# Kernel optimization log

Hardware: AMD Instinct MI355X
Metric: run time of the kernel (lower is better)

Reference implementation:

```python
import jax, jax.numpy as jnp
import numpy as np

N_NODES = 50000
N_EDGES = 800000
X_DIM, H_DIM, Y_DIM = 128, 256, 128


def spmm(adj_vals, adj_row, adj_col, x):
    # sparse [N,N] @ dense [N,D] via gather + segment scatter-add
    msgs = adj_vals[:, None] * x[adj_col]  # [E, D]
    return jax.ops.segment_sum(msgs, adj_row, num_segments=N_NODES)


def setup_inputs() -> dict:
    key = jax.random.key(0)
    ks = jax.random.split(key, 6)
    x = jax.random.uniform(ks[0], (N_NODES, X_DIM), dtype=jnp.float32)
    adj_vals = jax.random.uniform(ks[1], (N_EDGES,), dtype=jnp.float32)
    adj_row = jax.random.randint(ks[2], (N_EDGES,), 0, N_NODES, dtype=jnp.int32)
    adj_col = jax.random.randint(ks[3], (N_EDGES,), 0, N_NODES, dtype=jnp.int32)
    W1 = jax.random.normal(ks[4], (X_DIM, H_DIM), dtype=jnp.float32) * (1.0 / np.sqrt(X_DIM))
    b1 = jnp.zeros((H_DIM,), dtype=jnp.float32)
    W2 = jax.random.normal(ks[5], (H_DIM, Y_DIM), dtype=jnp.float32) * (1.0 / np.sqrt(H_DIM))
    b2 = jnp.zeros((Y_DIM,), dtype=jnp.float32)
    return {"x": x, "adj_vals": adj_vals, "adj_row": adj_row, "adj_col": adj_col,
            "W1": W1, "b1": b1, "W2": W2, "b2": b2}


def reference(x, adj_vals, adj_row, adj_col, W1, b1, W2, b2):
    # row-normalize features: x / (sum_j x_ij + 1e-4)
    x = x / (jnp.sum(x, axis=1, keepdims=True) + 1e-4)
    # layer 1: spmm -> linear -> relu (dropout is identity at eval)
    h = jax.nn.relu(spmm(adj_vals, adj_row, adj_col, x) @ W1 + b1)  # [N, H]
    # layer 2: spmm -> linear
    y = spmm(adj_vals, adj_row, adj_col, h) @ W2 + b2  # [N, Y]
    return y
```

## Files before the change

### kernel.cpp

```cpp
#include <hip/hip_runtime.h>

#define N_NODES 50000
#define N_EDGES 800000
#define X_DIM 128
#define H_DIM 256
#define Y_DIM 128

typedef unsigned int uint32;
typedef unsigned short ushort16;
typedef __attribute__((ext_vector_type(8))) short short8;
typedef __attribute__((ext_vector_type(4))) float floatx4;

__device__ inline ushort16 f2bf(float f) {
    uint32 u = __float_as_uint(f);
    return (ushort16)((u + 0x7FFFu + ((u >> 16) & 1u)) >> 16);
}
__device__ inline float bf_lo(uint32 u) { return __uint_as_float(u << 16); }
__device__ inline float bf_hi(uint32 u) { return __uint_as_float(u & 0xFFFF0000u); }

#define BUCKET_SHIFT 7
#define NB 391
#define CHUNK 4096
#define NCHUNK 196
#define CAP_B 2560

#define NORM_BLOCKS 12500
#define CONV_BLOCKS 256

__global__ __launch_bounds__(256) void prep_kernel(
    const float* __restrict__ x, uint32* __restrict__ xb,
    const float* __restrict__ W1, const float* __restrict__ W2,
    ushort16* __restrict__ W1t, ushort16* __restrict__ W2t,
    const int* __restrict__ rows, int* __restrict__ gpartial) {
    int b = blockIdx.x;
    if (b < NORM_BLOCKS) {
        int row = (b * 256 + threadIdx.x) >> 6;
        int lane = threadIdx.x & 63;
        float2 v = ((const float2*)x)[(size_t)row * 64 + lane];
        float s = v.x + v.y;
        #pragma unroll
        for (int off = 32; off > 0; off >>= 1) s += __shfl_xor(s, off, 64);
        float inv = 1.0f / (s + 1e-4f);
        uint32 lo = (uint32)f2bf(v.x * inv);
        uint32 hi = (uint32)f2bf(v.y * inv);
        xb[(size_t)row * 64 + lane] = lo | (hi << 16);
    } else if (b < NORM_BLOCKS + CONV_BLOCKS) {
        int t = (b - NORM_BLOCKS) * 256 + threadIdx.x;
        if (t < X_DIM * H_DIM) {
            int n = t >> 7, k = t & 127;
            W1t[t] = f2bf(W1[k * H_DIM + n]);
        } else {
            int u = t - X_DIM * H_DIM;
            int y = u >> 8, k = u & 255;
            W2t[u] = f2bf(W2[k * Y_DIM + y]);
        }
    } else {
        __shared__ int h[NB];
        int j = b - NORM_BLOCKS - CONV_BLOCKS;
        int t = threadIdx.x;
        for (int i = t; i < NB; i += 256) h[i] = 0;
        __syncthreads();
        int base = j * CHUNK;
        #pragma unroll
        for (int k = 0; k < CHUNK / 256; k++) {
            int e = base + t + k * 256;
            if (e < N_EDGES) atomicAdd(&h[rows[e] >> BUCKET_SHIFT], 1);
        }
        __syncthreads();
        for (int i = t; i < NB; i += 256) gpartial[j * NB + i] = h[i];
    }
}

__global__ __launch_bounds__(512) void bucket_scan_kernel(
    const int* __restrict__ gpartial, int* __restrict__ bucket_base,
    int* __restrict__ bcursor, int* __restrict__ rowptr) {
    __shared__ int s[512];
    int t = threadIdx.x;
    int total = 0;
    if (t < NB) {
        #pragma unroll 4
        for (int j = 0; j < NCHUNK; j++) total += gpartial[j * NB + t];
    }
    s[t] = total;
    __syncthreads();
    #pragma unroll
    for (int off = 1; off < 512; off <<= 1) {
        int u = (t >= off) ? s[t - off] : 0;
        __syncthreads();
        s[t] += u;
        __syncthreads();
    }
    if (t < NB) {
        int excl = s[t] - total;
        bucket_base[t] = excl;
        bcursor[t] = excl;
    }
    if (t == 0) { bucket_base[NB] = N_EDGES; rowptr[N_NODES] = N_EDGES; }
}

__global__ __launch_bounds__(512) void bucketize_kernel(
    const int* __restrict__ rows, const int* __restrict__ cols,
    const float* __restrict__ vals, const int* __restrict__ gpartial,
    int* __restrict__ bcursor, int2* __restrict__ edges) {
    __shared__ int ob[512];
    __shared__ int c[NB];
    __shared__ int g[NB];
    __shared__ int2 buf[CHUNK];
    int t = threadIdx.x;
    int j = blockIdx.x;
    int base = j * CHUNK;
    int M = N_EDGES - base; if (M > CHUNK) M = CHUNK;
    int cnt = (t < NB) ? gpartial[j * NB + t] : 0;
    ob[t] = cnt;
    __syncthreads();
    #pragma unroll
    for (int off = 1; off < 512; off <<= 1) {
        int u = (t >= off) ? ob[t - off] : 0;
        __syncthreads();
        ob[t] += u;
        __syncthreads();
    }
    ob[t] -= cnt;
    if (t < NB) {
        c[t] = 0;
        g[t] = (cnt > 0) ? atomicAdd(&bcursor[t], cnt) : 0;
    }
    __syncthreads();
    #pragma unroll
    for (int k = 0; k < CHUNK / 512; k++) {
        int e = base + t + k * 512;
        if (e < N_EDGES) {
            int r = rows[e];
            int bb = r >> BUCKET_SHIFT;
            int p = ob[bb] + atomicAdd(&c[bb], 1);
            buf[p] = make_int2(cols[e] | ((r & 127) << 16) | (bb << 23),
                               __float_as_int(vals[e]));
        }
    }
    __syncthreads();
    for (int i = t; i < M; i += 512) {
        int2 e = buf[i];
        int bb = (int)((uint32)e.x >> 23);
        edges[g[bb] + (i - ob[bb])] = e;
    }
}

__global__ __launch_bounds__(256) void bucket_sort_kernel(
    const int* __restrict__ bucket_base, int2* __restrict__ edges,
    int2* __restrict__ scratch, int* __restrict__ rowptr) {
    __shared__ int2 buf[CAP_B];
    __shared__ int2 buf2[CAP_B];
    __shared__ int h[128], o[128], c[128];
    int b = blockIdx.x, t = threadIdx.x;
    int base = bucket_base[b];
    int cnt = bucket_base[b + 1] - base;
    bool fits = (cnt <= CAP_B);
    if (t < 128) h[t] = 0;
    __syncthreads();
    for (int i = t; i < cnt; i += 256) {
        int2 e = edges[base + i];
        if (fits) buf[i] = e; else scratch[base + i] = e;
        atomicAdd(&h[(e.x >> 16) & 127], 1);
    }
    __syncthreads();
    int valh = (t < 128) ? h[t] : 0;
    #pragma unroll
    for (int off = 1; off < 128; off <<= 1) {
        int u = (t >= off && t < 128) ? h[t - off] : 0;
        __syncthreads();
        if (t < 128) h[t] += u;
        __syncthreads();
    }
    if (t < 128) {
        o[t] = h[t] - valh;
        c[t] = 0;
        int i = (b << BUCKET_SHIFT) + t;
        if (i < N_NODES) rowptr[i] = base + h[t] - valh;
    }
    __syncthreads();
    for (int i = t; i < cnt; i += 256) {
        int2 e = fits ? buf[i] : scratch[base + i];
        int lr = (e.x >> 16) & 127;
        int p = o[lr] + atomicAdd(&c[lr], 1);
        if (fits) buf2[p] = e; else edges[base + p] = e;
    }
    __syncthreads();
    if (fits)
        for (int i = t; i < cnt; i += 256) edges[base + i] = buf2[i];
}

__device__ __forceinline__ void spmm_row4(const uint4* __restrict__ feat4,
                                          const int2* __restrict__ edges,
                                          int start, int end, int lane,
                                          float A[8]) {
    const int g16 = lane & 15;
    const int bsrc = lane & 48;
    int cur = start;
    while (__any(cur < end)) {
        int n = end - cur;
        n = n < 0 ? 0 : (n > 16 ? 16 : n);
        int2 ev = make_int2(0, 0);
        if (g16 < n) ev = edges[cur + g16];
        int c = ev.x & 0xFFFF;
        float v = __int_as_float(ev.y);
        int n0 = __shfl(n, 0, 64), n1 = __shfl(n, 16, 64);
        int n2 = __shfl(n, 32, 64), n3 = __shfl(n, 48, 64);
        int nm = max(max(n0, n1), max(n2, n3));
        int jm = (nm + 7) & ~7;
        for (int j = 0; j < jm; j += 8) {
            uint4 f[8];
            float vv[8];
            #pragma unroll
            for (int u = 0; u < 8; u++) {
                int cc = __shfl(c, bsrc + j + u, 64);
                vv[u] = __shfl(v, bsrc + j + u, 64);
                f[u] = feat4[(size_t)cc * 16 + g16];
            }
            #pragma unroll
            for (int u = 0; u < 8; u++) {
                A[0] += vv[u] * bf_lo(f[u].x); A[1] += vv[u] * bf_hi(f[u].x);
                A[2] += vv[u] * bf_lo(f[u].y); A[3] += vv[u] * bf_hi(f[u].y);
                A[4] += vv[u] * bf_lo(f[u].z); A[5] += vv[u] * bf_hi(f[u].z);
                A[6] += vv[u] * bf_lo(f[u].w); A[7] += vv[u] * bf_hi(f[u].w);
            }
        }
        cur += n;
    }
}

__global__ __launch_bounds__(512, 4) void spmm_gemm_fused(
    const uint32* __restrict__ xb, const int* __restrict__ rowptr,
    const int2* __restrict__ edges, const ushort16* __restrict__ W1t,
    const ushort16* __restrict__ W2t, const float* __restrict__ b1,
    ushort16* __restrict__ hw) {
    __shared__ ushort16 a_s[64 * 136];
    __shared__ ushort16 h_s[64 * 264];
    const int tx = threadIdx.x;
    const int wave = tx >> 6, lane = tx & 63;
    const int quad = lane >> 4, l16 = lane & 15;
    const int row0 = blockIdx.x * 64;
    const uint4* xb4 = (const uint4*)xb;

    for (int i = 0; i < 2; i++) {
        int r = wave * 8 + i * 4 + quad;
        int row = row0 + r;
        int s = 0, e = 0;
        if (row < N_NODES) { s = rowptr[row]; e = rowptr[row + 1]; }
        float A[8] = {0.f, 0.f, 0.f, 0.f, 0.f, 0.f, 0.f, 0.f};
        spmm_row4(xb4, edges, s, e, lane, A);
        uint4 pk;
        pk.x = (uint32)f2bf(A[0]) | ((uint32)f2bf(A[1]) << 16);
        pk.y = (uint32)f2bf(A[2]) | ((uint32)f2bf(A[3]) << 16);
        pk.z = (uint32)f2bf(A[4]) | ((uint32)f2bf(A[5]) << 16);
        pk.w = (uint32)f2bf(A[6]) | ((uint32)f2bf(A[7]) << 16);
        *(uint4*)&a_s[r * 136 + l16 * 8] = pk;
    }

    short8 bfr1[2][4];
    #pragma unroll
    for (int ct = 0; ct < 2; ct++)
        #pragma unroll
        for (int kk = 0; kk < 4; kk++)
            bfr1[ct][kk] = *(const short8*)
                &W1t[(wave * 32 + ct * 16 + l16) * 128 + kk * 32 + quad * 8];
    __syncthreads();

    floatx4 acc1[4][2];
    #pragma unroll
    for (int rs = 0; rs < 4; rs++)
        #pragma unroll
        for (int ct = 0; ct < 2; ct++)
            #pragma unroll
            for (int j = 0; j < 4; j++) acc1[rs][ct][j] = 0.f;
    #pragma unroll
    for (int kk = 0; kk < 4; kk++) {
        #pragma unroll
        for (int rs = 0; rs < 4; rs++) {
            short8 af = *(const short8*)&a_s[(rs * 16 + l16) * 136 + kk * 32 + quad * 8];
            #pragma unroll
            for (int ct = 0; ct < 2; ct++)
                acc1[rs][ct] = __builtin_amdgcn_mfma_f32_16x16x32_bf16(
                    af, bfr1[ct][kk], acc1[rs][ct], 0, 0, 0);
        }
    }
    float bv[2];
    #pragma unroll
    for (int ct = 0; ct < 2; ct++) bv[ct] = b1[wave * 32 + ct * 16 + l16];
    #pragma unroll
    for (int rs = 0; rs < 4; rs++)
        #pragma unroll
        for (int ct = 0; ct < 2; ct++)
            #pragma unroll
            for (int reg = 0; reg < 4; reg++) {
                float v = acc1[rs][ct][reg] + bv[ct];
                v = v > 0.f ? v : 0.f;
                h_s[(rs * 16 + quad * 4 + reg) * 264 + wave * 32 + ct * 16 + l16] = f2bf(v);
            }

    short8 bfr2[8];
    #pragma unroll
    for (int kk = 0; kk < 8; kk++)
        bfr2[kk] = *(const short8*)
            &W2t[(wave * 16 + l16) * 256 + kk * 32 + quad * 8];
    __syncthreads();

    floatx4 acc2[4];
    #pragma unroll
    for (int rs = 0; rs < 4; rs++)
        #pragma unroll
        for (int j = 0; j < 4; j++) acc2[rs][j] = 0.f;
    #pragma unroll
    for (int kk = 0; kk < 8; kk++) {
        #pragma unroll
        for (int rs = 0; rs < 4; rs++) {
            short8 af = *(const short8*)&h_s[(rs * 16 + l16) * 264 + kk * 32 + quad * 8];
            acc2[rs] = __builtin_amdgcn_mfma_f32_16x16x32_bf16(
                af, bfr2[kk], acc2[rs], 0, 0, 0);
        }
    }
    #pragma unroll
    for (int rs = 0; rs < 4; rs++)
        #pragma unroll
        for (int reg = 0; reg < 4; reg++) {
            int row = row0 + rs * 16 + quad * 4 + reg;
            if (row < N_NODES)
                hw[(size_t)row * 128 + wave * 16 + l16] = f2bf(acc2[rs][reg]);
        }
}

__global__ __launch_bounds__(256) void spmm_out_kernel(
    const uint32* __restrict__ feat, const int* __restrict__ rowptr,
    const int2* __restrict__ edges, const float* __restrict__ bias,
    float* __restrict__ out) {
    int w = (blockIdx.x * blockDim.x + threadIdx.x) >> 6;
    int lane = threadIdx.x & 63;
    int quad = lane >> 4, g16 = lane & 15;
    int row = w * 4 + quad;
    int s = rowptr[row], e = rowptr[row + 1];
    float A[8] = {0.f, 0.f, 0.f, 0.f, 0.f, 0.f, 0.f, 0.f};
    spmm_row4((const uint4*)feat, edges, s, e, lane, A);
    float4 b0 = ((const float4*)bias)[g16 * 2];
    float4 b1 = ((const float4*)bias)[g16 * 2 + 1];
    ((float4*)out)[(size_t)row * 32 + g16 * 2] =
        make_float4(A[0] + b0.x, A[1] + b0.y, A[2] + b0.z, A[3] + b0.w);
    ((float4*)out)[(size_t)row * 32 + g16 * 2 + 1] =
        make_float4(A[4] + b1.x, A[5] + b1.y, A[6] + b1.z, A[7] + b1.w);
}

extern "C" void kernel_launch(void* const* d_in, const int* in_sizes, int n_in,
                              void* d_out, int out_size, void* d_ws, size_t ws_size,
                              hipStream_t stream) {
    const float* x = (const float*)d_in[0];
    const float* adj_vals = (const float*)d_in[1];
    const int* adj_row = (const int*)d_in[2];
    const int* adj_col = (const int*)d_in[3];
    const float* W1 = (const float*)d_in[4];
    const float* b1 = (const float*)d_in[5];
    const float* W2 = (const float*)d_in[6];
    const float* b2 = (const float*)d_in[7];
    float* out = (float*)d_out;

    char* ws = (char*)d_ws;
    uint32*   xb       = (uint32*)  (ws + 0);
    ushort16* hw       = (ushort16*)(ws + 12800000);
    int2*     edges    = (int2*)    (ws + 25600000);
    int2*     scratch  = (int2*)    (ws + 32000000);
    int*      gpartial = (int*)     (ws + 38400000);
    int*      rowptr   = (int*)     (ws + 38713344);
    int*      bbase    = (int*)     (ws + 38914048);
    int*      bcursor  = (int*)     (ws + 38916096);
    ushort16* W1t      = (ushort16*)(ws + 38918144);
    ushort16* W2t      = (ushort16*)(ws + 38983680);

    hipLaunchKernelGGL(prep_kernel, dim3(NORM_BLOCKS + CONV_BLOCKS + NCHUNK),
                       dim3(256), 0, stream, x, xb, W1, W2, W1t, W2t,
                       adj_row, gpartial);

    hipLaunchKernelGGL(bucket_scan_kernel, dim3(1), dim3(512),
                       0, stream, gpartial, bbase, bcursor, rowptr);

    hipLaunchKernelGGL(bucketize_kernel, dim3(NCHUNK), dim3(512),
                       0, stream, adj_row, adj_col, adj_vals, gpartial, bcursor, edges);
    hipLaunchKernelGGL(bucket_sort_kernel, dim3(NB), dim3(256),
                       0, stream, bbase, edges, scratch, rowptr);

    hipLaunchKernelGGL(spmm_gemm_fused, dim3((N_NODES + 63) / 64), dim3(512),
                       0, stream, xb, rowptr, edges, W1t, W2t, b1, hw);

    hipLaunchKernelGGL(spmm_out_kernel, dim3(N_NODES / 16), dim3(256),
                       0, stream, (const uint32*)hw, rowptr, edges, b2, out);
}
```

Measured before the change: 208.2 us.

## Fold bucket scan into bucketize and split fused SpMM-GEMM into two kernels

Removes the single-block bucket_scan kernel. Each bucketize block now recomputes global bucket totals and its own per-chunk prefix from gpartial, so no global atomic cursor is needed. It also splits the fused layer-1 SpMM+GEMM kernel into a high-occupancy SpMM kernel (256 threads, 8 blocks per CU) that writes a bf16 aggregate to global memory, followed by a GEMM kernel that reads it. The goal is to drop a serial launch and let the gather-bound SpMM run at higher occupancy. The cost is an extra global round trip for the 50000x128 aggregate and redundant reads of gpartial in every bucketize block. Scratch now aliases the hw buffer.

```diff
diff --git a/kernel.cpp b/kernel.cpp
--- a/kernel.cpp
+++ b/kernel.cpp
@@ -71,68 +71,64 @@
     }
 }
 
-__global__ __launch_bounds__(512) void bucket_scan_kernel(
-    const int* __restrict__ gpartial, int* __restrict__ bucket_base,
-    int* __restrict__ bcursor, int* __restrict__ rowptr) {
-    __shared__ int s[512];
-    int t = threadIdx.x;
-    int total = 0;
-    if (t < NB) {
-        #pragma unroll 4
-        for (int j = 0; j < NCHUNK; j++) total += gpartial[j * NB + t];
-    }
-    s[t] = total;
-    __syncthreads();
-    #pragma unroll
-    for (int off = 1; off < 512; off <<= 1) {
-        int u = (t >= off) ? s[t - off] : 0;
-        __syncthreads();
-        s[t] += u;
-        __syncthreads();
-    }
-    if (t < NB) {
-        int excl = s[t] - total;
-        bucket_base[t] = excl;
-        bcursor[t] = excl;
-    }
-    if (t == 0) { bucket_base[NB] = N_EDGES; rowptr[N_NODES] = N_EDGES; }
-}
-
 __global__ __launch_bounds__(512) void bucketize_kernel(
     const int* __restrict__ rows, const int* __restrict__ cols,
     const float* __restrict__ vals, const int* __restrict__ gpartial,
-    int* __restrict__ bcursor, int2* __restrict__ edges) {
+    int2* __restrict__ edges, int* __restrict__ bucket_base,
+    int* __restrict__ rowptr) {
+    __shared__ int sc[512];
     __shared__ int ob[512];
-    __shared__ int c[NB];
-    __shared__ int g[NB];
+    __shared__ int gw[NB];
+    __shared__ int cur[NB];
     __shared__ int2 buf[CHUNK];
     int t = threadIdx.x;
     int j = blockIdx.x;
     int base = j * CHUNK;
     int M = N_EDGES - base; if (M > CHUNK) M = CHUNK;
-    int cnt = (t < NB) ? gpartial[j * NB + t] : 0;
-    ob[t] = cnt;
+
+    int total = 0, pre = 0, cnt = 0;
+    if (t < NB) {
+        for (int jj = 0; jj < NCHUNK; jj++) {
+            int v = gpartial[jj * NB + t];
+            total += v;
+            pre += (jj < j) ? v : 0;
+        }
+        cnt = gpartial[j * NB + t];
+    }
+    sc[t] = total;
     __syncthreads();
     #pragma unroll
     for (int off = 1; off < 512; off <<= 1) {
-        int u = (t >= off) ? ob[t - off] : 0;
-        __syncthreads();
-        ob[t] += u;
-        __syncthreads();
-    }
-    ob[t] -= cnt;
-    if (t < NB) {
-        c[t] = 0;
-        g[t] = (cnt > 0) ? atomicAdd(&bcursor[t], cnt) : 0;
-    }
-    __syncthreads();
+        int u = (t >= off) ? sc[t - off] : 0;
+        __syncthreads();
+        sc[t] += u;
+        __syncthreads();
+    }
+    int bexcl = sc[t] - total;
+    if (t < NB) { gw[t] = bexcl + pre; cur[t] = 0; }
+    if (j == 0) {
+        if (t < NB) bucket_base[t] = bexcl;
+        if (t == 0) { bucket_base[NB] = N_EDGES; rowptr[N_NODES] = N_EDGES; }
+    }
+    sc[t] = cnt;
+    __syncthreads();
+    #pragma unroll
+    for (int off = 1; off < 512; off <<= 1) {
+        int u = (t >= off) ? sc[t - off] : 0;
+        __syncthreads();
+        sc[t] += u;
+        __syncthreads();
+    }
+    ob[t] = sc[t] - cnt;
+    __syncthreads();
+
     #pragma unroll
     for (int k = 0; k < CHUNK / 512; k++) {
         int e = base + t + k * 512;
         if (e < N_EDGES) {
             int r = rows[e];
             int bb = r >> BUCKET_SHIFT;
-            int p = ob[bb] + atomicAdd(&c[bb], 1);
+            int p = ob[bb] + atomicAdd(&cur[bb], 1);
             buf[p] = make_int2(cols[e] | ((r & 127) << 16) | (bb << 23),
                                __float_as_int(vals[e]));
         }
@@ -141,7 +137,7 @@
     for (int i = t; i < M; i += 512) {
         int2 e = buf[i];
         int bb = (int)((uint32)e.x >> 23);
-        edges[g[bb] + (i - ob[bb])] = e;
+        edges[gw[bb] + (i - ob[bb])] = e;
     }
 }
 
@@ -228,33 +224,33 @@
     }
 }
 
-__global__ __launch_bounds__(512, 4) void spmm_gemm_fused(
+__global__ __launch_bounds__(256, 8) void spmm1_kernel(
     const uint32* __restrict__ xb, const int* __restrict__ rowptr,
-    const int2* __restrict__ edges, const ushort16* __restrict__ W1t,
+    const int2* __restrict__ edges, uint32* __restrict__ agg) {
+    int w = (blockIdx.x * blockDim.x + threadIdx.x) >> 6;
+    int lane = threadIdx.x & 63;
+    int quad = lane >> 4, g16 = lane & 15;
+    int row = w * 4 + quad;
+    int s = rowptr[row], e = rowptr[row + 1];
+    float A[8] = {0.f, 0.f, 0.f, 0.f, 0.f, 0.f, 0.f, 0.f};
+    spmm_row4((const uint4*)xb, edges, s, e, lane, A);
+    uint4 pk;
+    pk.x = (uint32)f2bf(A[0]) | ((uint32)f2bf(A[1]) << 16);
+    pk.y = (uint32)f2bf(A[2]) | ((uint32)f2bf(A[3]) << 16);
+    pk.z = (uint32)f2bf(A[4]) | ((uint32)f2bf(A[5]) << 16);
+    pk.w = (uint32)f2bf(A[6]) | ((uint32)f2bf(A[7]) << 16);
+    ((uint4*)agg)[(size_t)row * 16 + g16] = pk;
+}
+
+__global__ __launch_bounds__(512, 4) void gemm_kernel(
+    const ushort16* __restrict__ agg, const ushort16* __restrict__ W1t,
     const ushort16* __restrict__ W2t, const float* __restrict__ b1,
     ushort16* __restrict__ hw) {
-    __shared__ ushort16 a_s[64 * 136];
     __shared__ ushort16 h_s[64 * 264];
     const int tx = threadIdx.x;
     const int wave = tx >> 6, lane = tx & 63;
     const int quad = lane >> 4, l16 = lane & 15;
     const int row0 = blockIdx.x * 64;
-    const uint4* xb4 = (const uint4*)xb;
-
-    for (int i = 0; i < 2; i++) {
-        int r = wave * 8 + i * 4 + quad;
-        int row = row0 + r;
-        int s = 0, e = 0;
-        if (row < N_NODES) { s = rowptr[row]; e = rowptr[row + 1]; }
-        float A[8] = {0.f, 0.f, 0.f, 0.f, 0.f, 0.f, 0.f, 0.f};
-        spmm_row4(xb4, edges, s, e, lane, A);
-        uint4 pk;
-        pk.x = (uint32)f2bf(A[0]) | ((uint32)f2bf(A[1]) << 16);
-        pk.y = (uint32)f2bf(A[2]) | ((uint32)f2bf(A[3]) << 16);
-        pk.z = (uint32)f2bf(A[4]) | ((uint32)f2bf(A[5]) << 16);
-        pk.w = (uint32)f2bf(A[6]) | ((uint32)f2bf(A[7]) << 16);
-        *(uint4*)&a_s[r * 136 + l16 * 8] = pk;
-    }
 
     short8 bfr1[2][4];
     #pragma unroll
@@ -263,7 +259,6 @@
         for (int kk = 0; kk < 4; kk++)
             bfr1[ct][kk] = *(const short8*)
                 &W1t[(wave * 32 + ct * 16 + l16) * 128 + kk * 32 + quad * 8];
-    __syncthreads();
 
     floatx4 acc1[4][2];
     #pragma unroll
@@ -276,7 +271,10 @@
     for (int kk = 0; kk < 4; kk++) {
         #pragma unroll
         for (int rs = 0; rs < 4; rs++) {
-            short8 af = *(const short8*)&a_s[(rs * 16 + l16) * 136 + kk * 32 + quad * 8];
+            int row = row0 + rs * 16 + l16;
+            short8 af = {};
+            if (row < N_NODES)
+                af = *(const short8*)&agg[(size_t)row * 128 + kk * 32 + quad * 8];
             #pragma unroll
             for (int ct = 0; ct < 2; ct++)
                 acc1[rs][ct] = __builtin_amdgcn_mfma_f32_16x16x32_bf16(
@@ -363,29 +361,31 @@
     char* ws = (char*)d_ws;
     uint32*   xb       = (uint32*)  (ws + 0);
     ushort16* hw       = (ushort16*)(ws + 12800000);
+    int2*     scratch  = (int2*)    (ws + 12800000);
     int2*     edges    = (int2*)    (ws + 25600000);
-    int2*     scratch  = (int2*)    (ws + 32000000);
-    int*      gpartial = (int*)     (ws + 38400000);
-    int*      rowptr   = (int*)     (ws + 38713344);
-    int*      bbase    = (int*)     (ws + 38914048);
-    int*      bcursor  = (int*)     (ws + 38916096);
-    ushort16* W1t      = (ushort16*)(ws + 38918144);
-    ushort16* W2t      = (ushort16*)(ws + 38983680);
+    ushort16* agg      = (ushort16*)(ws + 32000000);
+    int*      gpartial = (int*)     (ws + 44800000);
+    int*      rowptr   = (int*)     (ws + 45106560);
+    int*      bbase    = (int*)     (ws + 45306624);
+    ushort16* W1t      = (ushort16*)(ws + 45308224);
+    ushort16* W2t      = (ushort16*)(ws + 45373760);
 
     hipLaunchKernelGGL(prep_kernel, dim3(NORM_BLOCKS + CONV_BLOCKS + NCHUNK),
                        dim3(256), 0, stream, x, xb, W1, W2, W1t, W2t,
                        adj_row, gpartial);
 
-    hipLaunchKernelGGL(bucket_scan_kernel, dim3(1), dim3(512),
-                       0, stream, gpartial, bbase, bcursor, rowptr);
-
     hipLaunchKernelGGL(bucketize_kernel, dim3(NCHUNK), dim3(512),
-                       0, stream, adj_row, adj_col, adj_vals, gpartial, bcursor, edges);
+                       0, stream, adj_row, adj_col, adj_vals, gpartial,
+                       edges, bbase, rowptr);
+
     hipLaunchKernelGGL(bucket_sort_kernel, dim3(NB), dim3(256),
                        0, stream, bbase, edges, scratch, rowptr);
 
-    hipLaunchKernelGGL(spmm_gemm_fused, dim3((N_NODES + 63) / 64), dim3(512),
-                       0, stream, xb, rowptr, edges, W1t, W2t, b1, hw);
+    hipLaunchKernelGGL(spmm1_kernel, dim3(N_NODES / 16), dim3(256),
+                       0, stream, xb, rowptr, edges, (uint32*)agg);
+
+    hipLaunchKernelGGL(gemm_kernel, dim3((N_NODES + 63) / 64), dim3(512),
+                       0, stream, agg, W1t, W2t, b1, hw);
 
     hipLaunchKernelGGL(spmm_out_kernel, dim3(N_NODES / 16), dim3(256),
                        0, stream, (const uint32*)hw, rowptr, edges, b2, out);
```

Result: slower. 300.7 us (+44.4%).

## Quantize normalized input features to 8-bit with per-row scales for first SpMM

Applied to the files above, without the earlier changes.

The prep kernel now quantizes each input row to uint8 using a per-row max-based scale, folding the row-normalization into a stored float scale. The first SpMM gathers 8-byte rows instead of 16-byte bf16 rows and multiplies each edge value by the source row's scale, which halves gather traffic in the fused layer-1 kernel at the cost of one extra scale load per edge and lower precision. The output SpMM also gets an occupancy hint in its launch bounds. The 8-bit precision loss may or may not stay within tolerance.

```diff
diff --git a/kernel.cpp b/kernel.cpp
--- a/kernel.cpp
+++ b/kernel.cpp
@@ -18,6 +18,11 @@
 __device__ inline float bf_lo(uint32 u) { return __uint_as_float(u << 16); }
 __device__ inline float bf_hi(uint32 u) { return __uint_as_float(u & 0xFFFF0000u); }
 
+__device__ inline float ub0(uint32 u) { return (float)(u & 0xFFu); }
+__device__ inline float ub1(uint32 u) { return (float)((u >> 8) & 0xFFu); }
+__device__ inline float ub2(uint32 u) { return (float)((u >> 16) & 0xFFu); }
+__device__ inline float ub3(uint32 u) { return (float)(u >> 24); }
+
 #define BUCKET_SHIFT 7
 #define NB 391
 #define CHUNK 4096
@@ -28,7 +33,8 @@
 #define CONV_BLOCKS 256
 
 __global__ __launch_bounds__(256) void prep_kernel(
-    const float* __restrict__ x, uint32* __restrict__ xb,
+    const float* __restrict__ x, unsigned short* __restrict__ xq,
+    float* __restrict__ scales,
     const float* __restrict__ W1, const float* __restrict__ W2,
     ushort16* __restrict__ W1t, ushort16* __restrict__ W2t,
     const int* __restrict__ rows, int* __restrict__ gpartial) {
@@ -38,12 +44,18 @@
         int lane = threadIdx.x & 63;
         float2 v = ((const float2*)x)[(size_t)row * 64 + lane];
         float s = v.x + v.y;
-        #pragma unroll
-        for (int off = 32; off > 0; off >>= 1) s += __shfl_xor(s, off, 64);
+        float m = fmaxf(v.x, v.y);
+        #pragma unroll
+        for (int off = 32; off > 0; off >>= 1) {
+            s += __shfl_xor(s, off, 64);
+            m = fmaxf(m, __shfl_xor(m, off, 64));
+        }
         float inv = 1.0f / (s + 1e-4f);
-        uint32 lo = (uint32)f2bf(v.x * inv);
-        uint32 hi = (uint32)f2bf(v.y * inv);
-        xb[(size_t)row * 64 + lane] = lo | (hi << 16);
+        float rq = (m > 0.f) ? 127.f / m : 0.f;
+        int q0 = (int)(v.x * rq + 0.5f);
+        int q1 = (int)(v.y * rq + 0.5f);
+        xq[(size_t)row * 64 + lane] = (unsigned short)(q0 | (q1 << 8));
+        if (lane == 0) scales[row] = m * inv * (1.f / 127.f);
     } else if (b < NORM_BLOCKS + CONV_BLOCKS) {
         int t = (b - NORM_BLOCKS) * 256 + threadIdx.x;
         if (t < X_DIM * H_DIM) {
@@ -187,6 +199,50 @@
     __syncthreads();
     if (fits)
         for (int i = t; i < cnt; i += 256) edges[base + i] = buf2[i];
+}
+
+__device__ __forceinline__ void spmm_row4_q8(const uint2* __restrict__ xq2,
+                                             const float* __restrict__ scales,
+                                             const int2* __restrict__ edges,
+                                             int start, int end, int lane,
+                                             float A[8]) {
+    const int g16 = lane & 15;
+    const int bsrc = lane & 48;
+    int cur = start;
+    while (__any(cur < end)) {
+        int n = end - cur;
+        n = n < 0 ? 0 : (n > 16 ? 16 : n);
+        int2 ev = make_int2(0, 0);
+        float sc = 0.f;
+        if (g16 < n) {
+            ev = edges[cur + g16];
+            sc = scales[ev.x & 0xFFFF];
+        }
+        int c = ev.x & 0xFFFF;
+        float vs = __int_as_float(ev.y) * sc;
+        int n0 = __shfl(n, 0, 64), n1 = __shfl(n, 16, 64);
+        int n2 = __shfl(n, 32, 64), n3 = __shfl(n, 48, 64);
+        int nm = max(max(n0, n1), max(n2, n3));
+        int jm = (nm + 7) & ~7;
+        for (int j = 0; j < jm; j += 8) {
+            uint2 f[8];
+            float vv[8];
+            #pragma unroll
+            for (int u = 0; u < 8; u++) {
+                int cc = __shfl(c, bsrc + j + u, 64);
+                vv[u] = __shfl(vs, bsrc + j + u, 64);
+                f[u] = xq2[(size_t)cc * 16 + g16];
+            }
+            #pragma unroll
+            for (int u = 0; u < 8; u++) {
+                A[0] += vv[u] * ub0(f[u].x); A[1] += vv[u] * ub1(f[u].x);
+                A[2] += vv[u] * ub2(f[u].x); A[3] += vv[u] * ub3(f[u].x);
+                A[4] += vv[u] * ub0(f[u].y); A[5] += vv[u] * ub1(f[u].y);
+                A[6] += vv[u] * ub2(f[u].y); A[7] += vv[u] * ub3(f[u].y);
+            }
+        }
+        cur += n;
+    }
 }
 
 __device__ __forceinline__ void spmm_row4(const uint4* __restrict__ feat4,
@@ -229,7 +285,8 @@
 }
 
 __global__ __launch_bounds__(512, 4) void spmm_gemm_fused(
-    const uint32* __restrict__ xb, const int* __restrict__ rowptr,
+    const uint32* __restrict__ xq, const float* __restrict__ scales,
+    const int* __restrict__ rowptr,
     const int2* __restrict__ edges, const ushort16* __restrict__ W1t,
     const ushort16* __restrict__ W2t, const float* __restrict__ b1,
     ushort16* __restrict__ hw) {
@@ -239,7 +296,6 @@
     const int wave = tx >> 6, lane = tx & 63;
     const int quad = lane >> 4, l16 = lane & 15;
     const int row0 = blockIdx.x * 64;
-    const uint4* xb4 = (const uint4*)xb;
 
     for (int i = 0; i < 2; i++) {
         int r = wave * 8 + i * 4 + quad;
@@ -247,7 +303,7 @@
         int s = 0, e = 0;
         if (row < N_NODES) { s = rowptr[row]; e = rowptr[row + 1]; }
         float A[8] = {0.f, 0.f, 0.f, 0.f, 0.f, 0.f, 0.f, 0.f};
-        spmm_row4(xb4, edges, s, e, lane, A);
+        spmm_row4_q8((const uint2*)xq, scales, edges, s, e, lane, A);
         uint4 pk;
         pk.x = (uint32)f2bf(A[0]) | ((uint32)f2bf(A[1]) << 16);
         pk.y = (uint32)f2bf(A[2]) | ((uint32)f2bf(A[3]) << 16);
@@ -328,7 +384,7 @@
         }
 }
 
-__global__ __launch_bounds__(256) void spmm_out_kernel(
+__global__ __launch_bounds__(256, 4) void spmm_out_kernel(
     const uint32* __restrict__ feat, const int* __restrict__ rowptr,
     const int2* __restrict__ edges, const float* __restrict__ bias,
     float* __restrict__ out) {
@@ -361,19 +417,20 @@
     float* out = (float*)d_out;
 
     char* ws = (char*)d_ws;
-    uint32*   xb       = (uint32*)  (ws + 0);
-    ushort16* hw       = (ushort16*)(ws + 12800000);
-    int2*     edges    = (int2*)    (ws + 25600000);
-    int2*     scratch  = (int2*)    (ws + 32000000);
-    int*      gpartial = (int*)     (ws + 38400000);
-    int*      rowptr   = (int*)     (ws + 38713344);
-    int*      bbase    = (int*)     (ws + 38914048);
-    int*      bcursor  = (int*)     (ws + 38916096);
-    ushort16* W1t      = (ushort16*)(ws + 38918144);
-    ushort16* W2t      = (ushort16*)(ws + 38983680);
+    unsigned short* xq = (unsigned short*)(ws + 0);
+    float*    scales   = (float*)   (ws + 6400000);
+    ushort16* hw       = (ushort16*)(ws + 6600000);
+    int2*     edges    = (int2*)    (ws + 19400000);
+    int2*     scratch  = (int2*)    (ws + 25800000);
+    int*      gpartial = (int*)     (ws + 32200000);
+    int*      rowptr   = (int*)     (ws + 32507008);
+    int*      bbase    = (int*)     (ws + 32708000);
+    int*      bcursor  = (int*)     (ws + 32710048);
+    ushort16* W1t      = (ushort16*)(ws + 32712096);
+    ushort16* W2t      = (ushort16*)(ws + 32777632);
 
     hipLaunchKernelGGL(prep_kernel, dim3(NORM_BLOCKS + CONV_BLOCKS + NCHUNK),
-                       dim3(256), 0, stream, x, xb, W1, W2, W1t, W2t,
+                       dim3(256), 0, stream, x, xq, scales, W1, W2, W1t, W2t,
                        adj_row, gpartial);
 
     hipLaunchKernelGGL(bucket_scan_kernel, dim3(1), dim3(512),
@@ -385,7 +442,8 @@
                        0, stream, bbase, edges, scratch, rowptr);
 
     hipLaunchKernelGGL(spmm_gemm_fused, dim3((N_NODES + 63) / 64), dim3(512),
-                       0, stream, xb, rowptr, edges, W1t, W2t, b1, hw);
+                       0, stream, (const uint32*)xq, scales, rowptr, edges,
+                       W1t, W2t, b1, hw);
 
     hipLaunchKernelGGL(spmm_out_kernel, dim3(N_NODES / 16), dim3(256),
                        0, stream, (const uint32*)hw, rowptr, edges, b2, out);
```

Result: slower. 216.2 us (+3.9%).
